# Optimization experiments

Hardware: AMD Instinct MI355X
Metric: run time of the kernel (lower is better)

## Reference

```python
import jax, jax.numpy as jnp
import numpy as np

N_NODES = 50000
N_EDGES = 800000
IN_C, HID_C, OUT_C = 512, 256, 128


def setup_inputs() -> dict:
    key = jax.random.key(0)
    k1, k2, k3, k4, k5, k6 = jax.random.split(key, 6)
    x = jax.random.normal(k1, (N_NODES, IN_C), dtype=jnp.float32)
    edge_index = jax.random.randint(k2, (2, N_EDGES), 0, N_NODES, dtype=jnp.int64)
    # Glorot-ish init for linear weights, zero bias (PyG GCNConv default)
    W1 = jax.random.normal(k3, (IN_C, HID_C), dtype=jnp.float32) / np.sqrt(IN_C)
    b1 = jnp.zeros((HID_C,), dtype=jnp.float32)
    W2 = jax.random.normal(k4, (HID_C, OUT_C), dtype=jnp.float32) / np.sqrt(HID_C)
    b2 = jnp.zeros((OUT_C,), dtype=jnp.float32)
    return {"x": x, "edge_index": edge_index, "W1": W1, "b1": b1, "W2": W2, "b2": b2}


def _gcn_layer(h, src, dst, norm, W, b, n_nodes):
    # h: [N, Fin] -> [N, Fout];  out_i = sum_{j->i} norm_e * (h W)_j + b
    h = h @ W
    msg = h[src] * norm[:, None]            # [E+N, Fout]
    out = jax.ops.segment_sum(msg, dst, num_segments=n_nodes)
    return out + b


def reference(x, edge_index, W1, b1, W2, b2):
    n = x.shape[0]
    loops = jnp.arange(n, dtype=edge_index.dtype)
    src = jnp.concatenate([edge_index[0], loops])  # add self-loops
    dst = jnp.concatenate([edge_index[1], loops])
    # symmetric normalization D^{-1/2} (A+I) D^{-1/2}
    deg = jax.ops.segment_sum(jnp.ones_like(src, dtype=x.dtype), dst, num_segments=n)
    dinv = jax.lax.rsqrt(jnp.maximum(deg, 1.0))
    norm = dinv[src] * dinv[dst]

    h = _gcn_layer(x, src, dst, norm, W1, b1, n)
    h = jax.nn.relu(h)
    # dropout: identity in eval mode (training=False)
    out = _gcn_layer(h, src, dst, norm, W2, b2, n)
    return out
```

## Files before the change

kernel.cpp:

```cpp
#include <hip/hip_runtime.h>
#include <hip/hip_bf16.h>

#define N_NODES 50000
#define N_EDGES 800000
#define IN_C 512
#define HID_C 256
#define OUT_C 128
#define SCAN_BLOCKS 49

typedef short bf16x8 __attribute__((ext_vector_type(8)));
typedef float f32x4 __attribute__((ext_vector_type(4)));

__device__ __forceinline__ float bf2f(unsigned short u) {
    return __uint_as_float(((unsigned)u) << 16);
}
__device__ __forceinline__ unsigned short f2bf(float f) {
    __hip_bfloat16 h = __float2bfloat16(f);
    return *(unsigned short*)&h;
}

__global__ void zero_counts_kernel(int* __restrict__ counts) {
    int i = blockIdx.x * blockDim.x + threadIdx.x;
    if (i < N_NODES) counts[i] = 0;
}

__global__ void count_kernel(const int* __restrict__ ei, int* __restrict__ counts) {
    int e = blockIdx.x * blockDim.x + threadIdx.x;
    if (e < N_EDGES) atomicAdd(&counts[ei[N_EDGES + e]], 1);
}

__global__ __launch_bounds__(256) void scan_part_kernel(const int* __restrict__ counts,
                                                        int* __restrict__ excl,
                                                        int* __restrict__ bsums) {
    __shared__ int tsum[256];
    const int t = threadIdx.x;
    const int base = blockIdx.x * 1024 + t * 4;
    int v[4];
    int s = 0;
#pragma unroll
    for (int j = 0; j < 4; j++) {
        int idx = base + j;
        v[j] = (idx < N_NODES) ? counts[idx] : 0;
        s += v[j];
    }
    tsum[t] = s;
    __syncthreads();
    for (int off = 1; off < 256; off <<= 1) {
        int add = (t >= off) ? tsum[t - off] : 0;
        __syncthreads();
        tsum[t] += add;
        __syncthreads();
    }
    int run = tsum[t] - s;
#pragma unroll
    for (int j = 0; j < 4; j++) {
        int idx = base + j;
        if (idx < N_NODES) excl[idx] = run;
        run += v[j];
    }
    if (t == 255) bsums[blockIdx.x] = tsum[255];
}

__global__ void scan_sums_kernel(int* __restrict__ bsums) {
    int ln = threadIdx.x;
    int v = (ln < SCAN_BLOCKS) ? bsums[ln] : 0;
    for (int off = 1; off < 64; off <<= 1) {
        int u = __shfl_up(v, off, 64);
        if (ln >= off) v += u;
    }
    int excl = __shfl_up(v, 1, 64);
    if (ln == 0) excl = 0;
    if (ln < SCAN_BLOCKS) bsums[ln] = excl;
}

__global__ void add_dinv_kernel(int* __restrict__ offsets, const int* __restrict__ bsums,
                                int* __restrict__ woff, const int* __restrict__ counts,
                                float* __restrict__ dinv) {
    int i = blockIdx.x * blockDim.x + threadIdx.x;
    if (i < N_NODES) {
        int o = offsets[i] + bsums[i >> 10];
        offsets[i] = o;
        woff[i] = o;
        dinv[i] = rsqrtf(1.0f + (float)counts[i]);
    }
    if (i == 0) offsets[N_NODES] = N_EDGES;
}

__global__ void fill_kernel(const int* __restrict__ ei, int* __restrict__ woff,
                            const float* __restrict__ dinv,
                            int* __restrict__ sorted_src, float* __restrict__ sorted_w) {
    int e = blockIdx.x * blockDim.x + threadIdx.x;
    if (e < N_EDGES) {
        int s = ei[e];
        int d = ei[N_EDGES + e];
        int pos = atomicAdd(&woff[d], 1);
        sorted_src[pos] = s;
        sorted_w[pos] = dinv[s];
    }
}

__global__ __launch_bounds__(256) void cast_x_kernel(const float* __restrict__ x,
                                                     unsigned short* __restrict__ xb) {
    size_t i = ((size_t)blockIdx.x * 256 + threadIdx.x) * 4;
    float4 v = *(const float4*)&x[i];
    ushort4 o;
    o.x = f2bf(v.x); o.y = f2bf(v.y); o.z = f2bf(v.z); o.w = f2bf(v.w);
    *(ushort4*)&xb[i] = o;
}

__global__ __launch_bounds__(256) void tcast_kernel(const float* __restrict__ W,
                                                    unsigned short* __restrict__ WT,
                                                    int K, int N) {
    int idx = blockIdx.x * 256 + threadIdx.x;
    int n = idx / K, k = idx - n * K;
    WT[idx] = f2bf(W[(size_t)k * N + n]);
}

__global__ __launch_bounds__(256) void mfma_gemm_bt(const unsigned short* __restrict__ A,
                                                    const unsigned short* __restrict__ BT,
                                                    unsigned short* __restrict__ C,
                                                    int M, int N, int K) {
    __shared__ unsigned short As[128 * 32];
    __shared__ unsigned short Bs[128 * 32];

    const int tid = threadIdx.x;
    const int w = tid >> 6;
    const int ln = tid & 63;
    const int br = blockIdx.y * 128;
    const int bc = blockIdx.x * 128;

    const int quad = ln >> 4;
    const int l16 = ln & 15;
    const int wr = (w >> 1) * 64;
    const int wc = (w & 1) * 64;

    const int crow = ln >> 2;
    const int koff = (ln & 3) * 8;

    f32x4 acc[4][4];
#pragma unroll
    for (int mt = 0; mt < 4; mt++)
#pragma unroll
        for (int nt = 0; nt < 4; nt++) acc[mt][nt] = (f32x4){0.f, 0.f, 0.f, 0.f};

    for (int kk = 0; kk < K; kk += 32) {
#pragma unroll
        for (int t = 0; t < 2; t++) {
            int c = w + t * 4;
            int row = br + c * 16 + crow;
            row = row < M ? row : M - 1;
            const unsigned short* gp = A + (size_t)row * K + kk + koff;
            unsigned short* lp = As + c * 512 + ln * 8;
            __builtin_amdgcn_global_load_lds((const __attribute__((address_space(1))) void*)gp,
                                             (__attribute__((address_space(3))) void*)lp,
                                             16, 0, 0);
        }
#pragma unroll
        for (int t = 0; t < 2; t++) {
            int c = w + t * 4;
            int row = bc + c * 16 + crow;
            const unsigned short* gp = BT + (size_t)row * K + kk + koff;
            unsigned short* lp = Bs + c * 512 + ln * 8;
            __builtin_amdgcn_global_load_lds((const __attribute__((address_space(1))) void*)gp,
                                             (__attribute__((address_space(3))) void*)lp,
                                             16, 0, 0);
        }
        __syncthreads();

        bf16x8 af[4], bfr[4];
#pragma unroll
        for (int mt = 0; mt < 4; mt++)
            af[mt] = *(const bf16x8*)&As[(wr + mt * 16 + l16) * 32 + quad * 8];
#pragma unroll
        for (int nt = 0; nt < 4; nt++)
            bfr[nt] = *(const bf16x8*)&Bs[(wc + nt * 16 + l16) * 32 + quad * 8];
#pragma unroll
        for (int mt = 0; mt < 4; mt++)
#pragma unroll
            for (int nt = 0; nt < 4; nt++)
                acc[mt][nt] = __builtin_amdgcn_mfma_f32_16x16x32_bf16(af[mt], bfr[nt],
                                                                      acc[mt][nt], 0, 0, 0);
        __syncthreads();
    }

#pragma unroll
    for (int mt = 0; mt < 4; mt++) {
#pragma unroll
        for (int r = 0; r < 4; r++) {
            int gr = br + wr + mt * 16 + quad * 4 + r;
            if (gr < M) {
#pragma unroll
                for (int nt = 0; nt < 4; nt++) {
                    int gc = bc + wc + nt * 16 + l16;
                    C[(size_t)gr * N + gc] = f2bf(acc[mt][nt][r]);
                }
            }
        }
    }
}

template <int C, bool RELU, bool BF16_OUT>
__global__ __launch_bounds__(256) void gather_agg_kernel(const int* __restrict__ offsets,
                                                         const int* __restrict__ ssrc,
                                                         const float* __restrict__ sw,
                                                         const unsigned short* __restrict__ H,
                                                         const float* __restrict__ dinv,
                                                         const float* __restrict__ bias,
                                                         void* __restrict__ outv) {
    constexpr int G = C / 8;
    constexpr int NG = 64 / G;
    const int node = blockIdx.x * 4 + (threadIdx.x >> 6);
    if (node >= N_NODES) return;
    const int ln = threadIdx.x & 63;
    const int g = ln / G;
    const int l = ln % G;
    const int c0 = l * 8;
    const float di = dinv[node];

    float acc[8] = {};
    if (g == 0) {
        bf16x8 h = *(const bf16x8*)&H[(size_t)node * C + c0];
#pragma unroll
        for (int j = 0; j < 8; j++)
            acc[j] = di * di * bf2f((unsigned short)h[j]) + bias[c0 + j];
    }

    int k = offsets[node] + g;
    const int k1 = offsets[node + 1];
    for (; k + NG < k1; k += 2 * NG) {
        int s0 = ssrc[k], s1 = ssrc[k + NG];
        float w0 = di * sw[k], w1 = di * sw[k + NG];
        bf16x8 h0 = *(const bf16x8*)&H[(size_t)s0 * C + c0];
        bf16x8 h1 = *(const bf16x8*)&H[(size_t)s1 * C + c0];
#pragma unroll
        for (int j = 0; j < 8; j++)
            acc[j] += w0 * bf2f((unsigned short)h0[j]) + w1 * bf2f((unsigned short)h1[j]);
    }
    if (k < k1) {
        int s0 = ssrc[k];
        float w0 = di * sw[k];
        bf16x8 h0 = *(const bf16x8*)&H[(size_t)s0 * C + c0];
#pragma unroll
        for (int j = 0; j < 8; j++) acc[j] += w0 * bf2f((unsigned short)h0[j]);
    }

#pragma unroll
    for (int m = G; m < 64; m <<= 1) {
#pragma unroll
        for (int j = 0; j < 8; j++) acc[j] += __shfl_xor(acc[j], m, 64);
    }

    if (g == 0) {
        if (RELU) {
#pragma unroll
            for (int j = 0; j < 8; j++) acc[j] = fmaxf(acc[j], 0.0f);
        }
        if (BF16_OUT) {
            bf16x8 o;
#pragma unroll
            for (int j = 0; j < 8; j++) o[j] = (short)f2bf(acc[j]);
            *(bf16x8*)&((unsigned short*)outv)[(size_t)node * C + c0] = o;
        } else {
            float* out = (float*)outv;
            *(float4*)&out[(size_t)node * C + c0] = make_float4(acc[0], acc[1], acc[2], acc[3]);
            *(float4*)&out[(size_t)node * C + c0 + 4] = make_float4(acc[4], acc[5], acc[6], acc[7]);
        }
    }
}

extern "C" void kernel_launch(void* const* d_in, const int* in_sizes, int n_in,
                              void* d_out, int out_size, void* d_ws, size_t ws_size,
                              hipStream_t stream) {
    const float* x  = (const float*)d_in[0];
    const int*   ei = (const int*)d_in[1];
    const float* W1 = (const float*)d_in[2];
    const float* b1 = (const float*)d_in[3];
    const float* W2 = (const float*)d_in[4];
    const float* b2 = (const float*)d_in[5];
    float* out = (float*)d_out;

    int*   counts     = (int*)d_ws;
    int*   offsets    = counts + 50048;
    int*   woff       = offsets + 50052;
    int*   bsums      = woff + 50048;
    float* dinv       = (float*)(bsums + 64);
    int*   sorted_src = (int*)(dinv + 50048);
    float* sorted_w   = (float*)(sorted_src + 800000);
    unsigned short* W1T = (unsigned short*)(sorted_w + 800000);
    unsigned short* W2T = W1T + 131072;
    unsigned short* xb  = W2T + 32768;
    unsigned short* H1  = xb + (size_t)N_NODES * IN_C;
    unsigned short* A1b = xb;
    unsigned short* H2  = xb + (size_t)N_NODES * HID_C;

    zero_counts_kernel<<<(N_NODES + 255) / 256, 256, 0, stream>>>(counts);
    count_kernel<<<(N_EDGES + 255) / 256, 256, 0, stream>>>(ei, counts);
    scan_part_kernel<<<SCAN_BLOCKS, 256, 0, stream>>>(counts, offsets, bsums);
    scan_sums_kernel<<<1, 64, 0, stream>>>(bsums);
    add_dinv_kernel<<<(N_NODES + 255) / 256, 256, 0, stream>>>(offsets, bsums, woff, counts, dinv);
    fill_kernel<<<(N_EDGES + 255) / 256, 256, 0, stream>>>(ei, woff, dinv, sorted_src, sorted_w);

    cast_x_kernel<<<(N_NODES * IN_C) / 1024, 256, 0, stream>>>(x, xb);
    tcast_kernel<<<(IN_C * HID_C) / 256, 256, 0, stream>>>(W1, W1T, IN_C, HID_C);
    tcast_kernel<<<(HID_C * OUT_C) / 256, 256, 0, stream>>>(W2, W2T, HID_C, OUT_C);

    {
        dim3 grid(HID_C / 128, (N_NODES + 127) / 128);
        mfma_gemm_bt<<<grid, 256, 0, stream>>>(xb, W1T, H1, N_NODES, HID_C, IN_C);
    }
    gather_agg_kernel<HID_C, true, true><<<(N_NODES + 3) / 4, 256, 0, stream>>>(
        offsets, sorted_src, sorted_w, H1, dinv, b1, (void*)A1b);

    {
        dim3 grid(OUT_C / 128, (N_NODES + 127) / 128);
        mfma_gemm_bt<<<grid, 256, 0, stream>>>(A1b, W2T, H2, N_NODES, OUT_C, HID_C);
    }
    gather_agg_kernel<OUT_C, false, false><<<(N_NODES + 3) / 4, 256, 0, stream>>>(
        offsets, sorted_src, sorted_w, H2, dinv, b2, (void*)out);
}
```

Baseline: 428.7 us.

## Split gather aggregation into 32-channel slices and compute edge weights on the fly

The gather-aggregate kernel now has each block handle a 32-channel slice for 16 nodes, with 16 edges processed in parallel per node, instead of one wavefront covering a node's full channel width. Adjacent blocks cover different slices, so the gathered working set per pass is narrower and cache locality may improve. Per-edge weights are no longer precomputed into sorted_w; they are computed from dinv[src] at gather time, which removes the weight array write and read. The cost is an extra random dinv load per edge per slice, edge indices re-read once per slice, and the loss of the 2-way unrolled edge loop.

Measured after the change: 579.2 us. +35.1%, slower.

```diff
diff --git a/kernel.cpp b/kernel.cpp
--- a/kernel.cpp
+++ b/kernel.cpp
@@ -87,15 +87,13 @@
 }
 
 __global__ void fill_kernel(const int* __restrict__ ei, int* __restrict__ woff,
-                            const float* __restrict__ dinv,
-                            int* __restrict__ sorted_src, float* __restrict__ sorted_w) {
+                            int* __restrict__ sorted_src) {
     int e = blockIdx.x * blockDim.x + threadIdx.x;
     if (e < N_EDGES) {
         int s = ei[e];
         int d = ei[N_EDGES + e];
         int pos = atomicAdd(&woff[d], 1);
         sorted_src[pos] = s;
-        sorted_w[pos] = dinv[s];
     }
 }
 
@@ -200,70 +198,72 @@
 }
 
 template <int C, bool RELU, bool BF16_OUT>
-__global__ __launch_bounds__(256) void gather_agg_kernel(const int* __restrict__ offsets,
-                                                         const int* __restrict__ ssrc,
-                                                         const float* __restrict__ sw,
-                                                         const unsigned short* __restrict__ H,
-                                                         const float* __restrict__ dinv,
-                                                         const float* __restrict__ bias,
-                                                         void* __restrict__ outv) {
-    constexpr int G = C / 8;
-    constexpr int NG = 64 / G;
-    const int node = blockIdx.x * 4 + (threadIdx.x >> 6);
-    if (node >= N_NODES) return;
+__global__ __launch_bounds__(256) void gather_slice_kernel(
+    const int* __restrict__ offsets, const int* __restrict__ ssrc,
+    const unsigned short* __restrict__ H, const float* __restrict__ dinv,
+    const float* __restrict__ bias, void* __restrict__ outv) {
+    constexpr int NS = C / 32;
+    const int slice = blockIdx.x % NS;
+    const int chunk = blockIdx.x / NS;
+    const int w = threadIdx.x >> 6;
     const int ln = threadIdx.x & 63;
-    const int g = ln / G;
-    const int l = ln % G;
-    const int c0 = l * 8;
-    const float di = dinv[node];
-
-    float acc[8] = {};
-    if (g == 0) {
-        bf16x8 h = *(const bf16x8*)&H[(size_t)node * C + c0];
-#pragma unroll
-        for (int j = 0; j < 8; j++)
-            acc[j] = di * di * bf2f((unsigned short)h[j]) + bias[c0 + j];
-    }
-
-    int k = offsets[node] + g;
-    const int k1 = offsets[node + 1];
-    for (; k + NG < k1; k += 2 * NG) {
-        int s0 = ssrc[k], s1 = ssrc[k + NG];
-        float w0 = di * sw[k], w1 = di * sw[k + NG];
-        bf16x8 h0 = *(const bf16x8*)&H[(size_t)s0 * C + c0];
-        bf16x8 h1 = *(const bf16x8*)&H[(size_t)s1 * C + c0];
-#pragma unroll
-        for (int j = 0; j < 8; j++)
-            acc[j] += w0 * bf2f((unsigned short)h0[j]) + w1 * bf2f((unsigned short)h1[j]);
-    }
-    if (k < k1) {
-        int s0 = ssrc[k];
-        float w0 = di * sw[k];
-        bf16x8 h0 = *(const bf16x8*)&H[(size_t)s0 * C + c0];
-#pragma unroll
-        for (int j = 0; j < 8; j++) acc[j] += w0 * bf2f((unsigned short)h0[j]);
-    }
-
-#pragma unroll
-    for (int m = G; m < 64; m <<= 1) {
-#pragma unroll
-        for (int j = 0; j < 8; j++) acc[j] += __shfl_xor(acc[j], m, 64);
-    }
-
-    if (g == 0) {
-        if (RELU) {
-#pragma unroll
-            for (int j = 0; j < 8; j++) acc[j] = fmaxf(acc[j], 0.0f);
-        }
-        if (BF16_OUT) {
-            bf16x8 o;
-#pragma unroll
-            for (int j = 0; j < 8; j++) o[j] = (short)f2bf(acc[j]);
-            *(bf16x8*)&((unsigned short*)outv)[(size_t)node * C + c0] = o;
-        } else {
-            float* out = (float*)outv;
-            *(float4*)&out[(size_t)node * C + c0] = make_float4(acc[0], acc[1], acc[2], acc[3]);
-            *(float4*)&out[(size_t)node * C + c0 + 4] = make_float4(acc[4], acc[5], acc[6], acc[7]);
+    const int g = ln >> 2;
+    const int l = ln & 3;
+    const int c0 = slice * 32 + l * 8;
+
+    float bv[8];
+    {
+        float4 b0 = *(const float4*)&bias[c0];
+        float4 b1 = *(const float4*)&bias[c0 + 4];
+        bv[0] = b0.x; bv[1] = b0.y; bv[2] = b0.z; bv[3] = b0.w;
+        bv[4] = b1.x; bv[5] = b1.y; bv[6] = b1.z; bv[7] = b1.w;
+    }
+
+#pragma unroll
+    for (int t = 0; t < 4; t++) {
+        const int node = chunk * 16 + w * 4 + t;
+        if (node >= N_NODES) return;
+        const float di = dinv[node];
+
+        float acc[8] = {};
+        if (g == 0) {
+            bf16x8 h = *(const bf16x8*)&H[(size_t)node * C + c0];
+#pragma unroll
+            for (int j = 0; j < 8; j++)
+                acc[j] = di * di * bf2f((unsigned short)h[j]) + bv[j];
+        }
+
+        int k = offsets[node] + g;
+        const int k1 = offsets[node + 1];
+        for (; k < k1; k += 16) {
+            int s = ssrc[k];
+            float wgt = di * dinv[s];
+            bf16x8 h = *(const bf16x8*)&H[(size_t)s * C + c0];
+#pragma unroll
+            for (int j = 0; j < 8; j++) acc[j] += wgt * bf2f((unsigned short)h[j]);
+        }
+
+#pragma unroll
+        for (int m = 4; m < 64; m <<= 1) {
+#pragma unroll
+            for (int j = 0; j < 8; j++) acc[j] += __shfl_xor(acc[j], m, 64);
+        }
+
+        if (g == 0) {
+            if (RELU) {
+#pragma unroll
+                for (int j = 0; j < 8; j++) acc[j] = fmaxf(acc[j], 0.0f);
+            }
+            if (BF16_OUT) {
+                bf16x8 o;
+#pragma unroll
+                for (int j = 0; j < 8; j++) o[j] = (short)f2bf(acc[j]);
+                *(bf16x8*)&((unsigned short*)outv)[(size_t)node * C + c0] = o;
+            } else {
+                float* out = (float*)outv;
+                *(float4*)&out[(size_t)node * C + c0] = make_float4(acc[0], acc[1], acc[2], acc[3]);
+                *(float4*)&out[(size_t)node * C + c0 + 4] = make_float4(acc[4], acc[5], acc[6], acc[7]);
+            }
         }
     }
 }
@@ -285,8 +285,7 @@
     int*   bsums      = woff + 50048;
     float* dinv       = (float*)(bsums + 64);
     int*   sorted_src = (int*)(dinv + 50048);
-    float* sorted_w   = (float*)(sorted_src + 800000);
-    unsigned short* W1T = (unsigned short*)(sorted_w + 800000);
+    unsigned short* W1T = (unsigned short*)(sorted_src + 800000);
     unsigned short* W2T = W1T + 131072;
     unsigned short* xb  = W2T + 32768;
     unsigned short* H1  = xb + (size_t)N_NODES * IN_C;
@@ -298,7 +297,7 @@
     scan_part_kernel<<<SCAN_BLOCKS, 256, 0, stream>>>(counts, offsets, bsums);
     scan_sums_kernel<<<1, 64, 0, stream>>>(bsums);
     add_dinv_kernel<<<(N_NODES + 255) / 256, 256, 0, stream>>>(offsets, bsums, woff, counts, dinv);
-    fill_kernel<<<(N_EDGES + 255) / 256, 256, 0, stream>>>(ei, woff, dinv, sorted_src, sorted_w);
+    fill_kernel<<<(N_EDGES + 255) / 256, 256, 0, stream>>>(ei, woff, sorted_src);
 
     cast_x_kernel<<<(N_NODES * IN_C) / 1024, 256, 0, stream>>>(x, xb);
     tcast_kernel<<<(IN_C * HID_C) / 256, 256, 0, stream>>>(W1, W1T, IN_C, HID_C);
@@ -308,13 +307,13 @@
         dim3 grid(HID_C / 128, (N_NODES + 127) / 128);
         mfma_gemm_bt<<<grid, 256, 0, stream>>>(xb, W1T, H1, N_NODES, HID_C, IN_C);
     }
-    gather_agg_kernel<HID_C, true, true><<<(N_NODES + 3) / 4, 256, 0, stream>>>(
-        offsets, sorted_src, sorted_w, H1, dinv, b1, (void*)A1b);
+    gather_slice_kernel<HID_C, true, true><<<8 * 3125, 256, 0, stream>>>(
+        offsets, sorted_src, H1, dinv, b1, (void*)A1b);
 
     {
         dim3 grid(OUT_C / 128, (N_NODES + 127) / 128);
         mfma_gemm_bt<<<grid, 256, 0, stream>>>(A1b, W2T, H2, N_NODES, OUT_C, HID_C);
     }
-    gather_agg_kernel<OUT_C, false, false><<<(N_NODES + 3) / 4, 256, 0, stream>>>(
-        offsets, sorted_src, sorted_w, H2, dinv, b2, (void*)out);
-}
+    gather_slice_kernel<OUT_C, false, false><<<4 * 3125, 256, 0, stream>>>(
+        offsets, sorted_src, H2, dinv, b2, (void*)out);
+}
```
